# Optimization experiments

Hardware: AMD Instinct MI355X
Metric: run time of the kernel (lower is better)

## Reference

```python
import jax, jax.numpy as jnp
import numpy as np

N = 50000   # nodes
E = 800000  # edges (avg degree 16)
F = 128     # feature dim (input = hidden = output)
H = 8       # heads
D = F // H  # head dim = 16
L = 4       # layers


def setup_inputs() -> dict:
    key = jax.random.key(0)
    ks = jax.random.split(key, 11)
    x = jax.random.normal(ks[0], (N, F), dtype=jnp.float32)
    edge_index = jax.random.randint(ks[1], (2, E), 0, N, dtype=jnp.int64)
    s = 1.0 / np.sqrt(F)
    Wq = jax.random.normal(ks[2], (L, F, F), dtype=jnp.float32) * s
    Wk = jax.random.normal(ks[3], (L, F, F), dtype=jnp.float32) * s
    Wv = jax.random.normal(ks[4], (L, F, F), dtype=jnp.float32) * s
    Ws = jax.random.normal(ks[5], (L, F, F), dtype=jnp.float32) * s  # lin_skip (root weight)
    bq = jax.random.normal(ks[6], (L, F), dtype=jnp.float32) * 0.02
    bk = jax.random.normal(ks[7], (L, F), dtype=jnp.float32) * 0.02
    bv = jax.random.normal(ks[8], (L, F), dtype=jnp.float32) * 0.02
    bs = jax.random.normal(ks[9], (L, F), dtype=jnp.float32) * 0.02
    return {"x": x, "edge_index": edge_index, "Wq": Wq, "bq": bq,
            "Wk": Wk, "bk": bk, "Wv": Wv, "bv": bv, "Ws": Ws, "bs": bs}


def _transformer_conv(x, src, dst, Wq, bq, Wk, bk, Wv, bv, Ws, bs):
    # Q from destination nodes, K/V from source nodes (PyG TransformerConv).
    q = (x @ Wq + bq)[dst].reshape(E, H, D)
    k = (x @ Wk + bk)[src].reshape(E, H, D)
    alpha = (q * k).sum(-1) * (1.0 / np.sqrt(D))            # [E, H]
    # segment softmax over edges grouped by destination node
    amax = jax.ops.segment_max(alpha, dst, num_segments=N)   # [N, H]
    amax = jnp.where(jnp.isfinite(amax), amax, 0.0)
    p = jnp.exp(alpha - amax[dst])
    denom = jax.ops.segment_sum(p, dst, num_segments=N)      # [N, H]
    a = p / denom[dst]                                       # [E, H]
    v = (x @ Wv + bv)[src].reshape(E, H, D)
    msg = (a[..., None] * v).reshape(E, F)
    out = jax.ops.segment_sum(msg, dst, num_segments=N)      # concat heads
    out = out + x @ Ws + bs                                  # root/skip connection
    return out, a


def reference(x, edge_index, Wq, bq, Wk, bk, Wv, bv, Ws, bs):
    src, dst = edge_index[0], edge_index[1]
    alphas = []
    h = x
    for i in range(L - 1):
        h, a = _transformer_conv(h, src, dst, Wq[i], bq[i], Wk[i], bk[i],
                                 Wv[i], bv[i], Ws[i], bs[i])
        h = jax.nn.gelu(h, approximate=False)
        alphas.append(a)
    h, a = _transformer_conv(h, src, dst, Wq[-1], bq[-1], Wk[-1], bk[-1],
                             Wv[-1], bv[-1], Ws[-1], bs[-1])
    alphas.append(a)
    return h, jnp.stack(alphas)  # [N, F], [L, E, H]
```

## Files before the change

### kernel.cpp

```cpp
#include <hip/hip_runtime.h>
#include <math.h>

#define F 128
#define HEADS 8

typedef __attribute__((ext_vector_type(8))) short short8;
typedef __attribute__((ext_vector_type(4))) float floatx4;
typedef __attribute__((ext_vector_type(2))) _Float16 half2v;

__device__ __forceinline__ unsigned short f2bf(float f) {
    unsigned u = __float_as_uint(f);
    unsigned r = u + 0x7FFFu + ((u >> 16) & 1u);
    return (unsigned short)(r >> 16);
}

__device__ __forceinline__ half2v ashalf2(unsigned u) {
    return __builtin_bit_cast(half2v, u);
}
__device__ __forceinline__ unsigned pkh(float a, float b) {
    return __builtin_bit_cast(unsigned, __builtin_amdgcn_cvt_pkrtz(a, b));
}

#if __has_builtin(__builtin_amdgcn_fdot2)
#define FDOT2(a, b, c) __builtin_amdgcn_fdot2((a), (b), (c), false)
#else
#define FDOT2(a, b, c) ((c) + (float)(a)[0] * (float)(b)[0] + (float)(a)[1] * (float)(b)[1])
#endif


__global__ __launch_bounds__(256) void setup_k(
    const float* __restrict__ x, unsigned short* __restrict__ xb, int total4,
    const float* __restrict__ Wq, const float* __restrict__ Wk,
    const float* __restrict__ Wv, const float* __restrict__ Ws,
    unsigned short* __restrict__ wfrag, int wtotal,
    int* __restrict__ deg, int* __restrict__ cursor, int N) {
    int idx = blockIdx.x * 256 + threadIdx.x;
    if (idx < total4) {
        float4 v = ((const float4*)x)[idx];
        ushort4 o;
        o.x = f2bf(v.x); o.y = f2bf(v.y); o.z = f2bf(v.z); o.w = f2bf(v.w);
        ((ushort4*)xb)[idx] = o;
        return;
    }
    idx -= total4;
    if (idx < wtotal) {
        int j = idx & 7;
        int lane = (idx >> 3) & 63;
        int rest = idx >> 9;
        int chunk = rest & 3;
        int ftile = (rest >> 2) & 7;
        int mat = (rest >> 5) & 3;
        int layer = rest >> 7;
        int k = chunk * 32 + (lane >> 4) * 8 + j;
        int f = ftile * 16 + (lane & 15);
        const float* W = (mat == 0) ? Wq : (mat == 1) ? Wk : (mat == 2) ? Wv : Ws;
        wfrag[idx] = f2bf(W[((size_t)layer * F + k) * F + f]);
        return;
    }
    idx -= wtotal;
    if (idx < N) deg[idx] = 0;
    else if (idx < 2 * N) cursor[idx - N] = 0;
}


__global__ __launch_bounds__(256) void hist_k(const int* __restrict__ dst, int E, int* __restrict__ deg) {
    int e = blockIdx.x * 256 + threadIdx.x;
    if (e < E) atomicAdd(&deg[dst[e]], 1);
}

__global__ __launch_bounds__(256) void scan1_k(const int* __restrict__ deg, int N,
                                               int* __restrict__ start, int* __restrict__ partials) {
    __shared__ int sm[256];
    int t = threadIdx.x;
    int i = blockIdx.x * 256 + t;
    int v = (i < N) ? deg[i] : 0;
    sm[t] = v;
    __syncthreads();
    for (int off = 1; off < 256; off <<= 1) {
        int add = (t >= off) ? sm[t - off] : 0;
        __syncthreads();
        sm[t] += add;
        __syncthreads();
    }
    if (i < N) start[i] = sm[t] - v;
    if (t == 255) partials[blockIdx.x] = sm[t];
}

__global__ __launch_bounds__(256) void scan23_k(const int* __restrict__ partials, int nb,
                                                int* __restrict__ start, int N, int E) {
    __shared__ int sm[256];
    int t = threadIdx.x;
    int v = (t < nb) ? partials[t] : 0;
    sm[t] = v;
    __syncthreads();
    for (int off = 1; off < 256; off <<= 1) {
        int add = (t >= off) ? sm[t - off] : 0;
        __syncthreads();
        sm[t] += add;
        __syncthreads();
    }
    int myoff = sm[t] - v;
    __syncthreads();
    sm[t] = myoff;
    __syncthreads();
    for (int i = t; i < N; i += 256) start[i] += sm[i >> 8];
    if (t == 0) start[N] = E;
}

__global__ __launch_bounds__(256) void fill_k(const int* __restrict__ src, const int* __restrict__ dst, int E,
                                              const int* __restrict__ start, int* __restrict__ cursor,
                                              int2* __restrict__ epair) {
    int e = blockIdx.x * 256 + threadIdx.x;
    if (e < E) {
        int dd = dst[e];
        int pos = atomicAdd(&cursor[dd], 1);
        epair[start[dd] + pos] = make_int2(e, src[e]);
    }
}


__global__ __launch_bounds__(256) void gemm_mfma(
    const unsigned short* __restrict__ xb, const unsigned short* __restrict__ wfrag,
    const float* __restrict__ bq, const float* __restrict__ bk,
    const float* __restrict__ bv, const float* __restrict__ bs,
    unsigned short* __restrict__ Qh, unsigned short* __restrict__ KV,
    unsigned short* __restrict__ Sh, int N) {
    int wave = threadIdx.x >> 6;
    int lane = threadIdx.x & 63;
    int row0 = blockIdx.x * 32;
    int lm = lane & 15, quad = lane >> 4;
    const unsigned short* wf = wfrag + wave * 16384;

    floatx4 acc[2][8];
#pragma unroll
    for (int t = 0; t < 2; t++)
#pragma unroll
        for (int u = 0; u < 8; u++) acc[t][u] = (floatx4){0.f, 0.f, 0.f, 0.f};

#pragma unroll
    for (int chunk = 0; chunk < 4; chunk++) {
        short8 xfr[2];
#pragma unroll
        for (int t = 0; t < 2; t++) {
            int m = row0 + t * 16 + lm;
            m = (m < N) ? m : (N - 1);
            xfr[t] = *(const short8*)(xb + (size_t)m * F + chunk * 32 + quad * 8);
        }
#pragma unroll
        for (int u = 0; u < 8; u++) {
            short8 wfr = *(const short8*)(wf + ((u * 4 + chunk) * 64 + lane) * 8);
            acc[0][u] = __builtin_amdgcn_mfma_f32_16x16x32_bf16(wfr, xfr[0], acc[0][u], 0, 0, 0);
            acc[1][u] = __builtin_amdgcn_mfma_f32_16x16x32_bf16(wfr, xfr[1], acc[1][u], 0, 0, 0);
        }
    }

    const float* bias = (wave == 0) ? bq : (wave == 1) ? bk : (wave == 2) ? bv : bs;
    unsigned short* dp = (wave == 0) ? Qh : (wave == 3) ? Sh : KV;
    int kvwave = (wave == 1 || wave == 2);
    size_t rstride = kvwave ? 256 : 128;
    size_t roff = (wave == 2) ? 128 : 0;
#pragma unroll
    for (int u = 0; u < 8; u++) {
        float4 bv4 = *(const float4*)&bias[u * 16 + quad * 4];
#pragma unroll
        for (int t = 0; t < 2; t++) {
            int node = row0 + t * 16 + lm;
            if (node < N) {
                floatx4 a = acc[t][u];
                size_t off = (size_t)node * rstride + roff + u * 16 + quad * 4;
                *(uint2*)&dp[off] = make_uint2(pkh(a[0] + bv4.x, a[1] + bv4.y),
                                               pkh(a[2] + bv4.z, a[3] + bv4.w));
            }
        }
    }
}


__device__ __forceinline__ float gelu_exact(float v) {
    return 0.5f * v * (1.0f + erff(v * 0.70710678118654752f));
}

__global__ __launch_bounds__(256) void edge_k(
    const unsigned short* __restrict__ Qh, const unsigned short* __restrict__ KV,
    const unsigned short* __restrict__ Sh,
    const int* __restrict__ start, const int2* __restrict__ epair,
    float* __restrict__ aout,
    float* __restrict__ hout_f, unsigned short* __restrict__ hout_b,
    int N, int do_gelu) {
    __shared__ float wbuf[4][64][8];
    __shared__ int sbuf[4][64];
    __shared__ int ebuf[4][64];

    int wv = threadIdx.x >> 6;
    int lane = threadIdx.x & 63;
    int n = blockIdx.x * 4 + wv;
    if (n >= N) return;

    int beg = start[n], end = start[n + 1];
    int deg = end - beg;
    bool multi = deg > 64;
    int slot = lane >> 3, h = lane & 7;

    const unsigned short* qp = Qh + (size_t)n * F + h * 16;
    uint4 qa = *(const uint4*)(qp);
    uint4 qc = *(const uint4*)(qp + 8);
    half2v q0 = ashalf2(qa.x), q1 = ashalf2(qa.y), q2 = ashalf2(qa.z), q3 = ashalf2(qa.w);
    half2v q4 = ashalf2(qc.x), q5 = ashalf2(qc.y), q6 = ashalf2(qc.z), q7 = ashalf2(qc.w);

    float d = 0.f;
    float b0 = 0.f, b1 = 0.f, b2 = 0.f, b3 = 0.f, b4 = 0.f, b5 = 0.f, b6 = 0.f, b7 = 0.f;
    float b8 = 0.f, b9 = 0.f, b10 = 0.f, b11 = 0.f, b12 = 0.f, b13 = 0.f, b14 = 0.f, b15 = 0.f;

    for (int c0 = beg; c0 < end; c0 += 64) {
        int cnt = min(64, end - c0);

        int2 pe = epair[c0 + min(lane, cnt - 1)];
        sbuf[wv][lane] = pe.y << 9;
        ebuf[wv][lane] = pe.x;

        int nit = (cnt + 7) >> 3;
        for (int it = 0; it < nit; it++) {
            int idx = it * 8 + slot;
            bool val = idx < cnt;
            int ofs = sbuf[wv][val ? idx : 0];
            const unsigned short* kp = (const unsigned short*)((const char*)KV + ofs) + h * 16;
            uint4 ka = *(const uint4*)(kp);
            uint4 kc = *(const uint4*)(kp + 8);
            uint4 va = *(const uint4*)(kp + 128);
            uint4 vc = *(const uint4*)(kp + 136);
            float p0 = 0.f, p1 = 0.f;
            p0 = FDOT2(q0, ashalf2(ka.x), p0);
            p0 = FDOT2(q1, ashalf2(ka.y), p0);
            p0 = FDOT2(q2, ashalf2(ka.z), p0);
            p0 = FDOT2(q3, ashalf2(ka.w), p0);
            p1 = FDOT2(q4, ashalf2(kc.x), p1);
            p1 = FDOT2(q5, ashalf2(kc.y), p1);
            p1 = FDOT2(q6, ashalf2(kc.z), p1);
            p1 = FDOT2(q7, ashalf2(kc.w), p1);
            float w = __expf((p0 + p1) * 0.25f);
            if (!val) w = 0.f;
            d += w;
            wbuf[wv][idx][h] = w;
            if (multi && val) aout[(size_t)ebuf[wv][idx] * HEADS + h] = w;
            half2v x0 = ashalf2(va.x), x1 = ashalf2(va.y), x2 = ashalf2(va.z), x3 = ashalf2(va.w);
            half2v x4 = ashalf2(vc.x), x5 = ashalf2(vc.y), x6 = ashalf2(vc.z), x7 = ashalf2(vc.w);
            b0  += w * (float)x0[0]; b1  += w * (float)x0[1];
            b2  += w * (float)x1[0]; b3  += w * (float)x1[1];
            b4  += w * (float)x2[0]; b5  += w * (float)x2[1];
            b6  += w * (float)x3[0]; b7  += w * (float)x3[1];
            b8  += w * (float)x4[0]; b9  += w * (float)x4[1];
            b10 += w * (float)x5[0]; b11 += w * (float)x5[1];
            b12 += w * (float)x6[0]; b13 += w * (float)x6[1];
            b14 += w * (float)x7[0]; b15 += w * (float)x7[1];
        }
    }

    d += __shfl_xor(d, 8);
    d += __shfl_xor(d, 16);
    d += __shfl_xor(d, 32);
    float inv_d = (d > 0.f) ? 1.f / d : 0.f;

    if (!multi) {
        for (int idx = slot; idx < deg; idx += 8)
            aout[(size_t)ebuf[wv][idx] * HEADS + h] = wbuf[wv][idx][h] * inv_d;
    } else {
        for (int idx = slot; idx < deg; idx += 8)
            aout[(size_t)epair[beg + idx].x * HEADS + h] *= inv_d;
    }

    b0  += __shfl_xor(b0, 8);  b0  += __shfl_xor(b0, 16);  b0  += __shfl_xor(b0, 32);
    b1  += __shfl_xor(b1, 8);  b1  += __shfl_xor(b1, 16);  b1  += __shfl_xor(b1, 32);
    b2  += __shfl_xor(b2, 8);  b2  += __shfl_xor(b2, 16);  b2  += __shfl_xor(b2, 32);
    b3  += __shfl_xor(b3, 8);  b3  += __shfl_xor(b3, 16);  b3  += __shfl_xor(b3, 32);
    b4  += __shfl_xor(b4, 8);  b4  += __shfl_xor(b4, 16);  b4  += __shfl_xor(b4, 32);
    b5  += __shfl_xor(b5, 8);  b5  += __shfl_xor(b5, 16);  b5  += __shfl_xor(b5, 32);
    b6  += __shfl_xor(b6, 8);  b6  += __shfl_xor(b6, 16);  b6  += __shfl_xor(b6, 32);
    b7  += __shfl_xor(b7, 8);  b7  += __shfl_xor(b7, 16);  b7  += __shfl_xor(b7, 32);
    b8  += __shfl_xor(b8, 8);  b8  += __shfl_xor(b8, 16);  b8  += __shfl_xor(b8, 32);
    b9  += __shfl_xor(b9, 8);  b9  += __shfl_xor(b9, 16);  b9  += __shfl_xor(b9, 32);
    b10 += __shfl_xor(b10, 8); b10 += __shfl_xor(b10, 16); b10 += __shfl_xor(b10, 32);
    b11 += __shfl_xor(b11, 8); b11 += __shfl_xor(b11, 16); b11 += __shfl_xor(b11, 32);
    b12 += __shfl_xor(b12, 8); b12 += __shfl_xor(b12, 16); b12 += __shfl_xor(b12, 32);
    b13 += __shfl_xor(b13, 8); b13 += __shfl_xor(b13, 16); b13 += __shfl_xor(b13, 32);
    b14 += __shfl_xor(b14, 8); b14 += __shfl_xor(b14, 16); b14 += __shfl_xor(b14, 32);
    b15 += __shfl_xor(b15, 8); b15 += __shfl_xor(b15, 16); b15 += __shfl_xor(b15, 32);

    float* obuf = &wbuf[wv][0][0];
    asm volatile("s_waitcnt lgkmcnt(0)" ::: "memory");
    if (slot == 0) {
        *(float4*)&obuf[h * 16 + 0] = make_float4(b0 * inv_d, b1 * inv_d, b2 * inv_d, b3 * inv_d);
    } else if (slot == 1) {
        *(float4*)&obuf[h * 16 + 4] = make_float4(b4 * inv_d, b5 * inv_d, b6 * inv_d, b7 * inv_d);
    } else if (slot == 2) {
        *(float4*)&obuf[h * 16 + 8] = make_float4(b8 * inv_d, b9 * inv_d, b10 * inv_d, b11 * inv_d);
    } else if (slot == 3) {
        *(float4*)&obuf[h * 16 + 12] = make_float4(b12 * inv_d, b13 * inv_d, b14 * inv_d, b15 * inv_d);
    }
    asm volatile("s_waitcnt lgkmcnt(0)" ::: "memory");

    int f0 = lane * 2;
    float2 ov = *(const float2*)&obuf[f0];
    half2v s2 = ashalf2(*(const unsigned*)&Sh[(size_t)n * F + f0]);
    float o0 = ov.x + (float)s2[0];
    float o1 = ov.y + (float)s2[1];
    if (do_gelu) {
        o0 = gelu_exact(o0);
        o1 = gelu_exact(o1);
        unsigned ob = (unsigned)f2bf(o0) | ((unsigned)f2bf(o1) << 16);
        *(unsigned*)&hout_b[(size_t)n * F + f0] = ob;
    } else {
        *(float2*)&hout_f[(size_t)n * F + f0] = make_float2(o0, o1);
    }
}


extern "C" void kernel_launch(void* const* d_in, const int* in_sizes, int n_in,
                              void* d_out, int out_size, void* d_ws, size_t ws_size,
                              hipStream_t stream) {
    const float* x  = (const float*)d_in[0];
    const int*   ei = (const int*)d_in[1];
    const float* Wq = (const float*)d_in[2];
    const float* bq = (const float*)d_in[3];
    const float* Wk = (const float*)d_in[4];
    const float* bk = (const float*)d_in[5];
    const float* Wv = (const float*)d_in[6];
    const float* bv = (const float*)d_in[7];
    const float* Ws = (const float*)d_in[8];
    const float* bs = (const float*)d_in[9];

    const int N = in_sizes[0] / F;
    const int E = in_sizes[1] / 2;
    const int L = in_sizes[2] / (F * F);

    unsigned short* Sh = (unsigned short*)d_ws;
    unsigned short* Qh = Sh + (size_t)N * F;
    unsigned short* xb = Qh + (size_t)N * F;
    unsigned short* hb = xb + (size_t)N * F;
    unsigned short* KV = hb + (size_t)N * F;
    unsigned short* wfrag = KV + (size_t)N * 2 * F;
    int2* epair = (int2*)(wfrag + (size_t)L * 4 * 16384);
    int* start = (int*)(epair + E);
    int* cursor = start + (N + 1);
    int* deg = cursor + N;
    int* partials = deg + N;

    float* out_h = (float*)d_out;
    float* out_a = out_h + (size_t)N * F;

    const int* srcIdx = ei;
    const int* dstIdx = ei + E;

    int total4 = N * F / 4;
    int wtotal = L * 4 * 16384;
    int stotal = total4 + wtotal + 2 * N;
    setup_k<<<(stotal + 255) / 256, 256, 0, stream>>>(
        x, xb, total4, Wq, Wk, Wv, Ws, wfrag, wtotal, deg, cursor, N);

    int nbScan = (N + 255) / 256;
    hist_k<<<(E + 255) / 256, 256, 0, stream>>>(dstIdx, E, deg);
    scan1_k<<<nbScan, 256, 0, stream>>>(deg, N, start, partials);
    scan23_k<<<1, 256, 0, stream>>>(partials, nbScan, start, N, E);
    fill_k<<<(E + 255) / 256, 256, 0, stream>>>(srcIdx, dstIdx, E, start, cursor, epair);

    for (int l = 0; l < L; ++l) {
        const unsigned short* hin = (l == 0) ? xb : hb;
        gemm_mfma<<<(N + 31) / 32, 256, 0, stream>>>(
            hin, wfrag + (size_t)l * 4 * 16384,
            bq + (size_t)l * F, bk + (size_t)l * F,
            bv + (size_t)l * F, bs + (size_t)l * F,
            Qh, KV, Sh, N);
        edge_k<<<(N + 3) / 4, 256, 0, stream>>>(
            Qh, KV, Sh, start, epair,
            out_a + (size_t)l * E * HEADS, out_h, hb, N, (l < L - 1) ? 1 : 0);
    }
}
```

Before: 673.5 us.

## Split each node's edge aggregation across two waves with shared-memory combine

The edge kernel now assigns two wavefronts to each destination node instead of one. The waves interleave the edge chunks in groups of 8, then combine their softmax denominators and weighted-V partial sums through shared memory using block barriers. The aim is to shorten each wave's serial chain of dependent gathers and expose more memory-level parallelism for typical degree-16 nodes. In exchange it adds __syncthreads, redundant per-wave shuffle reductions, extra LDS traffic, and twice as many waves in the grid.

```diff
diff --git a/kernel.cpp b/kernel.cpp
--- a/kernel.cpp
+++ b/kernel.cpp
@@ -187,21 +187,26 @@
     float* __restrict__ aout,
     float* __restrict__ hout_f, unsigned short* __restrict__ hout_b,
     int N, int do_gelu) {
-    __shared__ float wbuf[4][64][8];
-    __shared__ int sbuf[4][64];
-    __shared__ int ebuf[4][64];
+    __shared__ float wbuf[2][64][8];
+    __shared__ int sbuf[2][2][64];
+    __shared__ int ebuf[2][2][64];
+    __shared__ float dbuf[2][2][8];
+    __shared__ float invdbuf[2][8];
+    __shared__ float obuf[2][2][128];
 
     int wv = threadIdx.x >> 6;
     int lane = threadIdx.x & 63;
-    int n = blockIdx.x * 4 + wv;
-    if (n >= N) return;
-
-    int beg = start[n], end = start[n + 1];
+    int pair = wv >> 1, w = wv & 1;
+    int n = blockIdx.x * 2 + pair;
+    bool nvalid = (n < N);
+    int nc = nvalid ? n : (N - 1);
+
+    int beg = start[nc], end = start[nc + 1];
     int deg = end - beg;
     bool multi = deg > 64;
     int slot = lane >> 3, h = lane & 7;
 
-    const unsigned short* qp = Qh + (size_t)n * F + h * 16;
+    const unsigned short* qp = Qh + (size_t)nc * F + h * 16;
     uint4 qa = *(const uint4*)(qp);
     uint4 qc = *(const uint4*)(qp + 8);
     half2v q0 = ashalf2(qa.x), q1 = ashalf2(qa.y), q2 = ashalf2(qa.z), q3 = ashalf2(qa.w);
@@ -215,14 +220,15 @@
         int cnt = min(64, end - c0);
 
         int2 pe = epair[c0 + min(lane, cnt - 1)];
-        sbuf[wv][lane] = pe.y << 9;
-        ebuf[wv][lane] = pe.x;
-
-        int nit = (cnt + 7) >> 3;
-        for (int it = 0; it < nit; it++) {
-            int idx = it * 8 + slot;
+        sbuf[pair][w][lane] = pe.y << 9;
+        ebuf[pair][w][lane] = pe.x;
+
+        int base = w * 8;
+        int nitw = (cnt > base) ? ((cnt - base + 15) >> 4) : 0;
+        for (int it = 0; it < nitw; it++) {
+            int idx = it * 16 + base + slot;
             bool val = idx < cnt;
-            int ofs = sbuf[wv][val ? idx : 0];
+            int ofs = sbuf[pair][w][val ? idx : 0];
             const unsigned short* kp = (const unsigned short*)((const char*)KV + ofs) + h * 16;
             uint4 ka = *(const uint4*)(kp);
             uint4 kc = *(const uint4*)(kp + 8);
@@ -237,35 +243,49 @@
             p1 = FDOT2(q5, ashalf2(kc.y), p1);
             p1 = FDOT2(q6, ashalf2(kc.z), p1);
             p1 = FDOT2(q7, ashalf2(kc.w), p1);
-            float w = __expf((p0 + p1) * 0.25f);
-            if (!val) w = 0.f;
-            d += w;
-            wbuf[wv][idx][h] = w;
-            if (multi && val) aout[(size_t)ebuf[wv][idx] * HEADS + h] = w;
+            float wcur = __expf((p0 + p1) * 0.25f);
+            if (!val) wcur = 0.f;
+            d += wcur;
+            wbuf[pair][idx][h] = wcur;
+            if (multi && val && nvalid) aout[(size_t)ebuf[pair][w][idx] * HEADS + h] = wcur;
             half2v x0 = ashalf2(va.x), x1 = ashalf2(va.y), x2 = ashalf2(va.z), x3 = ashalf2(va.w);
             half2v x4 = ashalf2(vc.x), x5 = ashalf2(vc.y), x6 = ashalf2(vc.z), x7 = ashalf2(vc.w);
-            b0  += w * (float)x0[0]; b1  += w * (float)x0[1];
-            b2  += w * (float)x1[0]; b3  += w * (float)x1[1];
-            b4  += w * (float)x2[0]; b5  += w * (float)x2[1];
-            b6  += w * (float)x3[0]; b7  += w * (float)x3[1];
-            b8  += w * (float)x4[0]; b9  += w * (float)x4[1];
-            b10 += w * (float)x5[0]; b11 += w * (float)x5[1];
-            b12 += w * (float)x6[0]; b13 += w * (float)x6[1];
-            b14 += w * (float)x7[0]; b15 += w * (float)x7[1];
+            b0  += wcur * (float)x0[0]; b1  += wcur * (float)x0[1];
+            b2  += wcur * (float)x1[0]; b3  += wcur * (float)x1[1];
+            b4  += wcur * (float)x2[0]; b5  += wcur * (float)x2[1];
+            b6  += wcur * (float)x3[0]; b7  += wcur * (float)x3[1];
+            b8  += wcur * (float)x4[0]; b9  += wcur * (float)x4[1];
+            b10 += wcur * (float)x5[0]; b11 += wcur * (float)x5[1];
+            b12 += wcur * (float)x6[0]; b13 += wcur * (float)x6[1];
+            b14 += wcur * (float)x7[0]; b15 += wcur * (float)x7[1];
         }
     }
 
     d += __shfl_xor(d, 8);
     d += __shfl_xor(d, 16);
     d += __shfl_xor(d, 32);
-    float inv_d = (d > 0.f) ? 1.f / d : 0.f;
-
-    if (!multi) {
-        for (int idx = slot; idx < deg; idx += 8)
-            aout[(size_t)ebuf[wv][idx] * HEADS + h] = wbuf[wv][idx][h] * inv_d;
-    } else {
-        for (int idx = slot; idx < deg; idx += 8)
-            aout[(size_t)epair[beg + idx].x * HEADS + h] *= inv_d;
+    if (slot == 0) dbuf[pair][w][h] = d;
+    __syncthreads();
+    float dtot = dbuf[pair][0][h] + dbuf[pair][1][h];
+    float inv_d = (dtot > 0.f) ? 1.f / dtot : 0.f;
+    if (w == 0 && slot == 0) invdbuf[pair][h] = inv_d;
+
+    if (nvalid) {
+        if (!multi) {
+            for (int it = 0;; it++) {
+                int ib = it * 16 + w * 8;
+                if (ib >= deg) break;
+                int idx = ib + slot;
+                if (idx < deg) aout[(size_t)ebuf[pair][w][idx] * HEADS + h] = wbuf[pair][idx][h] * inv_d;
+            }
+        } else {
+            for (int it = 0;; it++) {
+                int ib = it * 16 + w * 8;
+                if (ib >= deg) break;
+                int idx = ib + slot;
+                if (idx < deg) aout[(size_t)epair[beg + idx].x * HEADS + h] *= inv_d;
+            }
+        }
     }
 
     b0  += __shfl_xor(b0, 8);  b0  += __shfl_xor(b0, 16);  b0  += __shfl_xor(b0, 32);
@@ -285,31 +305,33 @@
     b14 += __shfl_xor(b14, 8); b14 += __shfl_xor(b14, 16); b14 += __shfl_xor(b14, 32);
     b15 += __shfl_xor(b15, 8); b15 += __shfl_xor(b15, 16); b15 += __shfl_xor(b15, 32);
 
-    float* obuf = &wbuf[wv][0][0];
-    asm volatile("s_waitcnt lgkmcnt(0)" ::: "memory");
     if (slot == 0) {
-        *(float4*)&obuf[h * 16 + 0] = make_float4(b0 * inv_d, b1 * inv_d, b2 * inv_d, b3 * inv_d);
+        *(float4*)&obuf[pair][w][h * 16 + 0] = make_float4(b0, b1, b2, b3);
     } else if (slot == 1) {
-        *(float4*)&obuf[h * 16 + 4] = make_float4(b4 * inv_d, b5 * inv_d, b6 * inv_d, b7 * inv_d);
+        *(float4*)&obuf[pair][w][h * 16 + 4] = make_float4(b4, b5, b6, b7);
     } else if (slot == 2) {
-        *(float4*)&obuf[h * 16 + 8] = make_float4(b8 * inv_d, b9 * inv_d, b10 * inv_d, b11 * inv_d);
+        *(float4*)&obuf[pair][w][h * 16 + 8] = make_float4(b8, b9, b10, b11);
     } else if (slot == 3) {
-        *(float4*)&obuf[h * 16 + 12] = make_float4(b12 * inv_d, b13 * inv_d, b14 * inv_d, b15 * inv_d);
-    }
-    asm volatile("s_waitcnt lgkmcnt(0)" ::: "memory");
-
-    int f0 = lane * 2;
-    float2 ov = *(const float2*)&obuf[f0];
-    half2v s2 = ashalf2(*(const unsigned*)&Sh[(size_t)n * F + f0]);
-    float o0 = ov.x + (float)s2[0];
-    float o1 = ov.y + (float)s2[1];
-    if (do_gelu) {
-        o0 = gelu_exact(o0);
-        o1 = gelu_exact(o1);
-        unsigned ob = (unsigned)f2bf(o0) | ((unsigned)f2bf(o1) << 16);
-        *(unsigned*)&hout_b[(size_t)n * F + f0] = ob;
-    } else {
-        *(float2*)&hout_f[(size_t)n * F + f0] = make_float2(o0, o1);
+        *(float4*)&obuf[pair][w][h * 16 + 12] = make_float4(b12, b13, b14, b15);
+    }
+    __syncthreads();
+
+    if (w == 0 && nvalid) {
+        int f0 = lane * 2;
+        float invd = invdbuf[pair][lane >> 3];
+        float t0 = (obuf[pair][0][f0] + obuf[pair][1][f0]) * invd;
+        float t1 = (obuf[pair][0][f0 + 1] + obuf[pair][1][f0 + 1]) * invd;
+        half2v s2 = ashalf2(*(const unsigned*)&Sh[(size_t)n * F + f0]);
+        float o0 = t0 + (float)s2[0];
+        float o1 = t1 + (float)s2[1];
+        if (do_gelu) {
+            o0 = gelu_exact(o0);
+            o1 = gelu_exact(o1);
+            unsigned ob = (unsigned)f2bf(o0) | ((unsigned)f2bf(o1) << 16);
+            *(unsigned*)&hout_b[(size_t)n * F + f0] = ob;
+        } else {
+            *(float2*)&hout_f[(size_t)n * F + f0] = make_float2(o0, o1);
+        }
     }
 }
 
@@ -369,7 +391,7 @@
             bq + (size_t)l * F, bk + (size_t)l * F,
             bv + (size_t)l * F, bs + (size_t)l * F,
             Qh, KV, Sh, N);
-        edge_k<<<(N + 3) / 4, 256, 0, stream>>>(
+        edge_k<<<(N + 1) / 2, 256, 0, stream>>>(
             Qh, KV, Sh, start, epair,
             out_a + (size_t)l * E * HEADS, out_h, hb, N, (l < L - 1) ? 1 : 0);
     }
```

Result: slower. 751.2 us (+11.5%).
